# Kernel optimization log

Measured on AMD Instinct MI355X. Metric: run time of the kernel, lower is better.

## Reference

```python
import jax, jax.numpy as jnp
import numpy as np

U = 512  # units

def hard_sigmoid(x):
    # Keras hard_sigmoid: clip(0.2*x + 0.5, 0, 1)
    return jnp.clip(0.2 * x + 0.5, 0.0, 1.0)

def setup_inputs() -> dict:
    key = jax.random.key(0)
    ks = jax.random.split(key, 9)
    B, T, A, D = 64, 2048, 512, 512  # batch, annotation steps, annotation units, input dim
    s = lambda k, shape, scale: jax.random.normal(k, shape, jnp.float32) * scale
    return {
        "inputs": s(ks[0], (B, D), 1.0),
        "h": s(ks[1], (B, U), 1.0),
        "c": s(ks[2], (B, U), 1.0),
        "annotations": s(ks[3], (B, T, A), 1.0),
        "kernel": s(ks[4], (D + A, 4 * U), 0.02),
        "recurrent_kernel": s(ks[5], (U, 4 * U), 0.02),
        "bias": jnp.zeros((6 * U,), jnp.float32).at[U:2 * U].set(1.0),  # unit_forget_bias
        "kernel_u": s(ks[6], (A, U), 0.02),
        "kernel_w": s(ks[7], (U, U), 0.02),
        "kernel_v": s(ks[8], (U,), 0.02),
    }

def reference(inputs, h, c, annotations, kernel, recurrent_kernel, bias, kernel_u, kernel_w, kernel_v):
    bias_u = bias[4 * U:5 * U]
    # precomputed annotation projection (done once in build()): [B,T,U]
    uh = jnp.einsum('bta,au->btu', annotations, kernel_u) + bias_u
    # Bahdanau attention scores
    Wxstm = h @ kernel_w                                   # [B,U]
    et = jnp.einsum('btu,u->bt', jnp.tanh(uh + Wxstm[:, None, :]), kernel_v)
    at = jax.nn.softmax(et, axis=1)                        # exp/sum in source == softmax
    context = jnp.einsum('bt,bta->ba', at, annotations)    # [B,A]
    x = jnp.concatenate([inputs, context], axis=-1)        # [B, D+A]
    z = x @ kernel + h @ recurrent_kernel + bias[:4 * U]   # [B,4U]
    i = hard_sigmoid(z[:, :U])
    f = hard_sigmoid(z[:, U:2 * U])
    c_new = f * c + i * jnp.tanh(z[:, 2 * U:3 * U])
    o = hard_sigmoid(z[:, 3 * U:])
    h_new = o * jnp.tanh(c_new)
    return h_new
```

## Files before the change

### kernel.cpp

```cpp
#include <hip/hip_runtime.h>

constexpr int U = 512;
constexpr int B = 64;
constexpr int T = 2048;
constexpr int A = 512;

typedef __attribute__((ext_vector_type(8))) short short8;
typedef __attribute__((ext_vector_type(4))) float f32x4;

__device__ __forceinline__ unsigned short f32_to_bf16(float f) {
    unsigned int b = __float_as_uint(f);
    unsigned int r = (b + 0x7FFFu + ((b >> 16) & 1u)) >> 16;
    return (unsigned short)r;
}

__device__ __forceinline__ float fast_tanh(float x) {
    float e = exp2f(x * 2.885390081777927f);
    return (e - 1.0f) * __builtin_amdgcn_rcpf(e + 1.0f);
}

__device__ __forceinline__ float hard_sigmoid(float z) {
    return fminf(fmaxf(0.2f * z + 0.5f, 0.0f), 1.0f);
}

__global__ __launch_bounds__(256) void k_prep_s(const float* __restrict__ h,
                                                const float* __restrict__ kw,
                                                float* __restrict__ Sp) {
    int b = blockIdx.x >> 2;
    int kc = blockIdx.x & 3;
    int u = threadIdx.x;
    const float* hb = h + b * U + kc * 128;
    const float* kwb = kw + (size_t)kc * 128 * U;
    float a0 = 0.f, a1 = 0.f;
#pragma unroll 4
    for (int k = 0; k < 128; ++k) {
        float hv = hb[k];
        a0 += hv * kwb[(size_t)k * U + u];
        a1 += hv * kwb[(size_t)k * U + u + 256];
    }
    float* p = Sp + ((size_t)kc * 64 + b) * U;
    p[u] = a0;
    p[u + 256] = a1;
}

__global__ __launch_bounds__(256) void k_s_reduce(const float* __restrict__ Sp,
                                                  const float* __restrict__ bias,
                                                  float* __restrict__ S) {
    int gid = blockIdx.x * 256 + threadIdx.x;
    int b = gid >> 9, u = gid & 511;
    float s = bias[4 * U + u];
#pragma unroll
    for (int kc = 0; kc < 4; ++kc) s += Sp[((size_t)kc * 64 + b) * U + u];
    S[gid] = s;
}

__global__ __launch_bounds__(256) void k_prep_kut(const float* __restrict__ ku,
                                                  unsigned short* __restrict__ kut) {
    __shared__ float tile[32][33];
    int a0 = (blockIdx.x >> 4) << 5;
    int u0 = (blockIdx.x & 15) << 5;
    int c = threadIdx.x & 31, r0 = threadIdx.x >> 5;
#pragma unroll
    for (int p = 0; p < 4; ++p) {
        int r = r0 + p * 8;
        tile[r][c] = ku[(a0 + r) * U + u0 + c];
    }
    __syncthreads();
#pragma unroll
    for (int p = 0; p < 4; ++p) {
        int r = r0 + p * 8;
        kut[(u0 + r) * A + a0 + c] = f32_to_bf16(tile[c][r]);
    }
}

__global__ __launch_bounds__(256) void k_prep_wt(const float* __restrict__ kern,
                                                 const float* __restrict__ rk,
                                                 unsigned short* __restrict__ Wt) {
    __shared__ float tile[32][33];
    int k0 = blockIdx.x << 5;
    int j0 = blockIdx.y << 5;
    int c = threadIdx.x & 31, r0 = threadIdx.x >> 5;
#pragma unroll
    for (int p = 0; p < 4; ++p) {
        int r = r0 + p * 8;
        int k = k0 + r;
        float val = (k < 1024) ? kern[k * 2048 + j0 + c]
                               : rk[(k - 1024) * 2048 + j0 + c];
        tile[r][c] = val;
    }
    __syncthreads();
#pragma unroll
    for (int p = 0; p < 4; ++p) {
        int r = r0 + p * 8;
        Wt[(size_t)(j0 + r) * 1536 + k0 + c] = f32_to_bf16(tile[c][r]);
    }
}

__global__ __launch_bounds__(256, 2) void k_gemm_et(const float* __restrict__ ann,
                                                    const unsigned short* __restrict__ kut,
                                                    const float* __restrict__ S,
                                                    const float* __restrict__ v,
                                                    float* __restrict__ et) {
    __shared__ unsigned short As[2][64 * 32];
    __shared__ unsigned short Bs[2][512 * 32];
    __shared__ float red[4][64];

    const int tid = threadIdx.x;
    const int wave = tid >> 6;
    const int lane = tid & 63;
    const int lanelo = lane & 15;
    const int quad = lane >> 4;
    const int wn = wave;

    const int mt = blockIdx.x;
    const int b = mt >> 5;
    const int t0 = (mt & 31) << 6;
    const float* aBase = ann + (size_t)mt * 64 * A;

    f32x4 acc[4][8];
#pragma unroll
    for (int i = 0; i < 4; ++i)
#pragma unroll
        for (int j = 0; j < 8; ++j) acc[i][j] = {0.f, 0.f, 0.f, 0.f};

    const int rowA = tid >> 2;
    const int c8A = tid & 3;
    f32x4 pv0, pv1;

    {
        const float* src = aBase + (size_t)rowA * A + 0 + c8A * 8;
        pv0 = *(const f32x4*)src;
        pv1 = *(const f32x4*)(src + 4);
    }
#pragma unroll
    for (int p = 0; p < 8; ++p) {
        int seg = p * 4 + wave;
        int flat = seg * 1024 + lane * 16;
        int row = flat >> 6;
        int sc = (flat >> 4) & 3;
        int d = sc ^ ((row >> 1) & 3);
        __builtin_amdgcn_global_load_lds(
            (const __attribute__((address_space(1))) void*)(kut + (size_t)row * A + 0 + d * 8),
            (__attribute__((address_space(3))) void*)((char*)&Bs[0][0] + seg * 1024),
            16, 0, 0);
    }
    {
        short8 pk;
        pk[0] = (short)f32_to_bf16(pv0.x);
        pk[1] = (short)f32_to_bf16(pv0.y);
        pk[2] = (short)f32_to_bf16(pv0.z);
        pk[3] = (short)f32_to_bf16(pv0.w);
        pk[4] = (short)f32_to_bf16(pv1.x);
        pk[5] = (short)f32_to_bf16(pv1.y);
        pk[6] = (short)f32_to_bf16(pv1.z);
        pk[7] = (short)f32_to_bf16(pv1.w);
        *(short8*)&As[0][rowA * 32 + ((c8A ^ ((rowA >> 1) & 3)) * 8)] = pk;
    }
    __syncthreads();

    for (int t = 0; t < 16; ++t) {
        const int cur = t & 1;
        const int nxt = cur ^ 1;
        const bool more = (t < 15);
        const int k1 = (t + 1) * 32;

        if (more) {
            const float* src = aBase + (size_t)rowA * A + k1 + c8A * 8;
            pv0 = *(const f32x4*)src;
            pv1 = *(const f32x4*)(src + 4);
#pragma unroll
            for (int p = 0; p < 8; ++p) {
                int seg = p * 4 + wave;
                int flat = seg * 1024 + lane * 16;
                int row = flat >> 6;
                int sc = (flat >> 4) & 3;
                int d = sc ^ ((row >> 1) & 3);
                __builtin_amdgcn_global_load_lds(
                    (const __attribute__((address_space(1))) void*)(kut + (size_t)row * A + k1 + d * 8),
                    (__attribute__((address_space(3))) void*)((char*)&Bs[nxt][0] + seg * 1024),
                    16, 0, 0);
            }
        }

        short8 af[4];
#pragma unroll
        for (int mi = 0; mi < 4; ++mi) {
            int row = mi * 16 + lanelo;
            af[mi] = *(const short8*)&As[cur][row * 32 + ((quad ^ ((row >> 1) & 3)) * 8)];
        }
        short8 bfr[8];
#pragma unroll
        for (int ni = 0; ni < 8; ++ni) {
            int rowb = wn * 128 + ni * 16 + lanelo;
            bfr[ni] = *(const short8*)&Bs[cur][rowb * 32 + ((quad ^ ((rowb >> 1) & 3)) * 8)];
        }
        __builtin_amdgcn_s_setprio(1);
#pragma unroll
        for (int mi = 0; mi < 4; ++mi)
#pragma unroll
            for (int ni = 0; ni < 8; ++ni)
                acc[mi][ni] = __builtin_amdgcn_mfma_f32_16x16x32_bf16(
                    af[mi], bfr[ni], acc[mi][ni], 0, 0, 0);
        __builtin_amdgcn_s_setprio(0);

        if (more) {
            short8 pk;
            pk[0] = (short)f32_to_bf16(pv0.x);
            pk[1] = (short)f32_to_bf16(pv0.y);
            pk[2] = (short)f32_to_bf16(pv0.z);
            pk[3] = (short)f32_to_bf16(pv0.w);
            pk[4] = (short)f32_to_bf16(pv1.x);
            pk[5] = (short)f32_to_bf16(pv1.y);
            pk[6] = (short)f32_to_bf16(pv1.z);
            pk[7] = (short)f32_to_bf16(pv1.w);
            *(short8*)&As[nxt][rowA * 32 + ((c8A ^ ((rowA >> 1) & 3)) * 8)] = pk;
        }
        __syncthreads();
    }

    float rows[16];
#pragma unroll
    for (int i = 0; i < 16; ++i) rows[i] = 0.f;
#pragma unroll
    for (int ni = 0; ni < 8; ++ni) {
        int u = wn * 128 + ni * 16 + lanelo;
        float sv = S[b * U + u];
        float vv = v[u];
#pragma unroll
        for (int mi = 0; mi < 4; ++mi)
#pragma unroll
            for (int r = 0; r < 4; ++r)
                rows[mi * 4 + r] += fast_tanh(acc[mi][ni][r] + sv) * vv;
    }
#pragma unroll
    for (int i = 0; i < 16; ++i) {
        rows[i] += __shfl_xor(rows[i], 1);
        rows[i] += __shfl_xor(rows[i], 2);
        rows[i] += __shfl_xor(rows[i], 4);
        rows[i] += __shfl_xor(rows[i], 8);
    }
    if (lanelo == 0) {
#pragma unroll
        for (int mi = 0; mi < 4; ++mi)
#pragma unroll
            for (int r = 0; r < 4; ++r)
                red[wave][mi * 16 + quad * 4 + r] = rows[mi * 4 + r];
    }
    __syncthreads();
    if (tid < 64) {
        float sum = red[0][tid] + red[1][tid] + red[2][tid] + red[3][tid];
        et[b * T + t0 + tid] = sum;
    }
}

__global__ __launch_bounds__(256) void k_softmax(const float* __restrict__ et,
                                                 float* __restrict__ at) {
    __shared__ float sred[256];
    int b = blockIdx.x;
    const float* e = et + b * T;
    float vals[8];
    float mx = -1e30f;
#pragma unroll
    for (int i = 0; i < 8; ++i) {
        int t = threadIdx.x + i * 256;
        float x = e[t];
        vals[i] = x;
        mx = fmaxf(mx, x);
    }
    sred[threadIdx.x] = mx;
    __syncthreads();
    for (int s = 128; s > 0; s >>= 1) {
        if (threadIdx.x < s) sred[threadIdx.x] = fmaxf(sred[threadIdx.x], sred[threadIdx.x + s]);
        __syncthreads();
    }
    mx = sred[0];
    __syncthreads();
    float sum = 0.f;
#pragma unroll
    for (int i = 0; i < 8; ++i) {
        float x = exp2f((vals[i] - mx) * 1.4426950408889634f);
        vals[i] = x;
        sum += x;
    }
    sred[threadIdx.x] = sum;
    __syncthreads();
    for (int s = 128; s > 0; s >>= 1) {
        if (threadIdx.x < s) sred[threadIdx.x] += sred[threadIdx.x + s];
        __syncthreads();
    }
    float inv = 1.0f / sred[0];
#pragma unroll
    for (int i = 0; i < 8; ++i) at[b * T + threadIdx.x + i * 256] = vals[i] * inv;
}

__global__ __launch_bounds__(256) void k_ctx_part(const float* __restrict__ at,
                                                  const float* __restrict__ ann,
                                                  float* __restrict__ part) {
    __shared__ float buf[2][512];
    int b = blockIdx.x >> 3;
    int tc = blockIdx.x & 7;
    int half = threadIdx.x >> 7;
    int a4 = (threadIdx.x & 127) << 2;
    const float* annb = ann + ((size_t)b * T + tc * 256) * A;
    const float* atb = at + b * T + tc * 256;
    f32x4 acc = {0.f, 0.f, 0.f, 0.f};
    for (int t = half; t < 256; t += 2) {
        float w = atb[t];
        f32x4 rv = *(const f32x4*)(annb + (size_t)t * A + a4);
        acc.x += w * rv.x;
        acc.y += w * rv.y;
        acc.z += w * rv.z;
        acc.w += w * rv.w;
    }
    *(f32x4*)&buf[half][a4] = acc;
    __syncthreads();
    int a2 = threadIdx.x << 1;
    float s0 = buf[0][a2] + buf[1][a2];
    float s1 = buf[0][a2 + 1] + buf[1][a2 + 1];
    float* p = part + ((size_t)b * 8 + tc) * A;
    p[a2] = s0;
    p[a2 + 1] = s1;
}

__global__ __launch_bounds__(256) void k_ctx_xb(const float* __restrict__ part,
                                                const float* __restrict__ inputs,
                                                const float* __restrict__ h,
                                                unsigned short* __restrict__ xb) {
    int b = blockIdx.x;
    unsigned short* xrow = xb + (size_t)b * 1536;
#pragma unroll
    for (int i = 0; i < 2; ++i) {
        int a = threadIdx.x + i * 256;
        float s = 0.f;
#pragma unroll
        for (int c = 0; c < 8; ++c) s += part[((size_t)b * 8 + c) * A + a];
        xrow[512 + a] = f32_to_bf16(s);
        xrow[a] = f32_to_bf16(inputs[b * 512 + a]);
        xrow[1024 + a] = f32_to_bf16(h[b * 512 + a]);
    }
}

__global__ __launch_bounds__(256) void k_zgemm(const unsigned short* __restrict__ xb,
                                               const unsigned short* __restrict__ Wt,
                                               float* __restrict__ zpart) {
    const int kc = blockIdx.x & 7;
    const int nt = blockIdx.x >> 3;
    const int wave = threadIdx.x >> 6;
    const int lane = threadIdx.x & 63;
    const int lanelo = lane & 15;
    const int quad = lane >> 4;

    const int n = nt * 64 + wave * 16 + lanelo;
    const unsigned short* bp = Wt + (size_t)n * 1536 + kc * 192 + quad * 8;
    const unsigned short* ap = xb + (size_t)lanelo * 1536 + kc * 192 + quad * 8;

    f32x4 acc[4];
#pragma unroll
    for (int i = 0; i < 4; ++i) acc[i] = {0.f, 0.f, 0.f, 0.f};

#pragma unroll
    for (int ks = 0; ks < 6; ++ks) {
        short8 bfrag = *(const short8*)(bp + ks * 32);
#pragma unroll
        for (int mi = 0; mi < 4; ++mi) {
            short8 afrag = *(const short8*)(ap + (size_t)mi * 16 * 1536 + ks * 32);
            acc[mi] = __builtin_amdgcn_mfma_f32_16x16x32_bf16(afrag, bfrag, acc[mi], 0, 0, 0);
        }
    }

    float* p = zpart + (size_t)kc * 64 * 2048;
#pragma unroll
    for (int mi = 0; mi < 4; ++mi)
#pragma unroll
        for (int r = 0; r < 4; ++r) {
            int m = mi * 16 + quad * 4 + r;
            p[(size_t)m * 2048 + n] = acc[mi][r];
        }
}

__global__ __launch_bounds__(256) void k_gates(const float* __restrict__ zpart,
                                               const float* __restrict__ bias,
                                               const float* __restrict__ c,
                                               float* __restrict__ hnew) {
    int gid = blockIdx.x * 256 + threadIdx.x;
    int b = gid >> 9;
    int u = gid & 511;
    float z[4];
#pragma unroll
    for (int g = 0; g < 4; ++g) {
        int j = (g << 9) + u;
        float s = bias[j];
#pragma unroll
        for (int kc = 0; kc < 8; ++kc)
            s += zpart[((size_t)kc * 64 + b) * 2048 + j];
        z[g] = s;
    }
    float ig = hard_sigmoid(z[0]);
    float fg = hard_sigmoid(z[1]);
    float cn = fg * c[b * 512 + u] + ig * fast_tanh(z[2]);
    float og = hard_sigmoid(z[3]);
    hnew[b * 512 + u] = og * fast_tanh(cn);
}

extern "C" void kernel_launch(void* const* d_in, const int* in_sizes, int n_in,
                              void* d_out, int out_size, void* d_ws, size_t ws_size,
                              hipStream_t stream) {
    const float* inputs = (const float*)d_in[0];
    const float* h      = (const float*)d_in[1];
    const float* c      = (const float*)d_in[2];
    const float* ann    = (const float*)d_in[3];
    const float* kern   = (const float*)d_in[4];
    const float* rk     = (const float*)d_in[5];
    const float* bias   = (const float*)d_in[6];
    const float* ku     = (const float*)d_in[7];
    const float* kw     = (const float*)d_in[8];
    const float* kv     = (const float*)d_in[9];

    char* ws = (char*)d_ws;
    float*          S     = (float*)(ws + 0);
    unsigned short* kut   = (unsigned short*)(ws + 131072);
    float*          et    = (float*)(ws + 655360);
    float*          at    = (float*)(ws + 1703936);
    float*          part  = (float*)(ws + 2228224);
    float*          Sp    = (float*)(ws + 2228224);
    unsigned short* xb    = (unsigned short*)(ws + 3407872);
    unsigned short* Wt    = (unsigned short*)(ws + 3604480);
    float*          zpart = (float*)(ws + 9895936);
    float*          hnew  = (float*)d_out;

    k_prep_wt<<<dim3(48, 64), 256, 0, stream>>>(kern, rk, Wt);
    k_prep_kut<<<256, 256, 0, stream>>>(ku, kut);
    k_prep_s<<<256, 256, 0, stream>>>(h, kw, Sp);
    k_s_reduce<<<128, 256, 0, stream>>>(Sp, bias, S);
    k_gemm_et<<<2048, 256, 0, stream>>>(ann, kut, S, kv, et);
    k_softmax<<<64, 256, 0, stream>>>(et, at);
    k_ctx_part<<<64 * 8, 256, 0, stream>>>(at, ann, part);
    k_ctx_xb<<<64, 256, 0, stream>>>(part, inputs, h, xb);
    k_zgemm<<<256, 256, 0, stream>>>(xb, Wt, zpart);
    k_gates<<<128, 256, 0, stream>>>(zpart, bias, c, hnew);
}
```

Before: 544.8 us.

## Enlarge attention GEMM tile to 128 rows with triple-buffered B pipeline

```diff
diff --git a/kernel.cpp b/kernel.cpp
--- a/kernel.cpp
+++ b/kernel.cpp
@@ -96,26 +96,26 @@
     }
 }
 
-__global__ __launch_bounds__(256, 2) void k_gemm_et(const float* __restrict__ ann,
+__global__ __launch_bounds__(512, 1) void k_gemm_et(const float* __restrict__ ann,
                                                     const unsigned short* __restrict__ kut,
                                                     const float* __restrict__ S,
                                                     const float* __restrict__ v,
                                                     float* __restrict__ et) {
-    __shared__ unsigned short As[2][64 * 32];
-    __shared__ unsigned short Bs[2][512 * 32];
-    __shared__ float red[4][64];
+    __shared__ unsigned short As[2][128 * 40];
+    __shared__ unsigned short Bs[3][512 * 32];
+    __shared__ float red[8][64];
 
     const int tid = threadIdx.x;
     const int wave = tid >> 6;
     const int lane = tid & 63;
     const int lanelo = lane & 15;
     const int quad = lane >> 4;
-    const int wn = wave;
+    const int wr = wave >> 2;
+    const int wc = wave & 3;
 
     const int mt = blockIdx.x;
-    const int b = mt >> 5;
-    const int t0 = (mt & 31) << 6;
-    const float* aBase = ann + (size_t)mt * 64 * A;
+    const int b = mt >> 4;
+    const float* aBase = ann + (size_t)mt * 128 * A;
 
     f32x4 acc[4][8];
 #pragma unroll
@@ -127,24 +127,22 @@
     const int c8A = tid & 3;
     f32x4 pv0, pv1;
 
-    {
-        const float* src = aBase + (size_t)rowA * A + 0 + c8A * 8;
-        pv0 = *(const f32x4*)src;
-        pv1 = *(const f32x4*)(src + 4);
-    }
-#pragma unroll
-    for (int p = 0; p < 8; ++p) {
-        int seg = p * 4 + wave;
-        int flat = seg * 1024 + lane * 16;
-        int row = flat >> 6;
-        int sc = (flat >> 4) & 3;
-        int d = sc ^ ((row >> 1) & 3);
-        __builtin_amdgcn_global_load_lds(
-            (const __attribute__((address_space(1))) void*)(kut + (size_t)row * A + 0 + d * 8),
-            (__attribute__((address_space(3))) void*)((char*)&Bs[0][0] + seg * 1024),
-            16, 0, 0);
-    }
-    {
+    auto stage_b = [&](int kk, int buf) {
+#pragma unroll
+        for (int p = 0; p < 4; ++p) {
+            int seg = p * 8 + wave;
+            int flat = seg * 1024 + lane * 16;
+            int row = flat >> 6;
+            int sc = (flat >> 4) & 3;
+            int d = sc ^ ((row >> 1) & 3);
+            __builtin_amdgcn_global_load_lds(
+                (const __attribute__((address_space(1))) void*)(kut + (size_t)row * A + kk + d * 8),
+                (__attribute__((address_space(3))) void*)((char*)&Bs[buf][0] + seg * 1024),
+                16, 0, 0);
+        }
+    };
+
+    auto cvt_store = [&](int buf) {
         short8 pk;
         pk[0] = (short)f32_to_bf16(pv0.x);
         pk[1] = (short)f32_to_bf16(pv0.y);
@@ -154,46 +152,55 @@
         pk[5] = (short)f32_to_bf16(pv1.y);
         pk[6] = (short)f32_to_bf16(pv1.z);
         pk[7] = (short)f32_to_bf16(pv1.w);
-        *(short8*)&As[0][rowA * 32 + ((c8A ^ ((rowA >> 1) & 3)) * 8)] = pk;
-    }
-    __syncthreads();
-
+        *(short8*)&As[buf][rowA * 40 + c8A * 8] = pk;
+    };
+
+    {
+        const float* src = aBase + (size_t)rowA * A + c8A * 8;
+        pv0 = *(const f32x4*)src;
+        pv1 = *(const f32x4*)(src + 4);
+    }
+    __builtin_amdgcn_sched_barrier(0);
+    stage_b(0, 0);
+    __builtin_amdgcn_sched_barrier(0);
+    asm volatile("s_waitcnt vmcnt(4)" ::: "memory");
+    cvt_store(0);
+    __builtin_amdgcn_sched_barrier(0);
+    stage_b(32, 1);
+    __builtin_amdgcn_sched_barrier(0);
+    asm volatile("s_waitcnt vmcnt(4)" ::: "memory");
+    asm volatile("s_waitcnt lgkmcnt(0)" ::: "memory");
+    __builtin_amdgcn_s_barrier();
+
+#pragma unroll
     for (int t = 0; t < 16; ++t) {
         const int cur = t & 1;
-        const int nxt = cur ^ 1;
-        const bool more = (t < 15);
-        const int k1 = (t + 1) * 32;
-
-        if (more) {
-            const float* src = aBase + (size_t)rowA * A + k1 + c8A * 8;
+        const int curB = t % 3;
+
+        __builtin_amdgcn_sched_barrier(0);
+        if (t < 15) {
+            const float* src = aBase + (size_t)rowA * A + (t + 1) * 32 + c8A * 8;
             pv0 = *(const f32x4*)src;
             pv1 = *(const f32x4*)(src + 4);
-#pragma unroll
-            for (int p = 0; p < 8; ++p) {
-                int seg = p * 4 + wave;
-                int flat = seg * 1024 + lane * 16;
-                int row = flat >> 6;
-                int sc = (flat >> 4) & 3;
-                int d = sc ^ ((row >> 1) & 3);
-                __builtin_amdgcn_global_load_lds(
-                    (const __attribute__((address_space(1))) void*)(kut + (size_t)row * A + k1 + d * 8),
-                    (__attribute__((address_space(3))) void*)((char*)&Bs[nxt][0] + seg * 1024),
-                    16, 0, 0);
-            }
-        }
+        }
+        __builtin_amdgcn_sched_barrier(0);
+        if (t < 14) stage_b((t + 2) * 32, (t + 2) % 3);
+        __builtin_amdgcn_sched_barrier(0);
 
         short8 af[4];
 #pragma unroll
         for (int mi = 0; mi < 4; ++mi) {
-            int row = mi * 16 + lanelo;
-            af[mi] = *(const short8*)&As[cur][row * 32 + ((quad ^ ((row >> 1) & 3)) * 8)];
+            int row = wr * 64 + mi * 16 + lanelo;
+            af[mi] = *(const short8*)&As[cur][row * 40 + quad * 8];
         }
         short8 bfr[8];
 #pragma unroll
         for (int ni = 0; ni < 8; ++ni) {
-            int rowb = wn * 128 + ni * 16 + lanelo;
-            bfr[ni] = *(const short8*)&Bs[cur][rowb * 32 + ((quad ^ ((rowb >> 1) & 3)) * 8)];
-        }
+            int rowb = wc * 128 + ni * 16 + lanelo;
+            int ch = quad ^ ((rowb >> 1) & 3);
+            bfr[ni] = *(const short8*)&Bs[curB][rowb * 32 + ch * 8];
+        }
+
         __builtin_amdgcn_s_setprio(1);
 #pragma unroll
         for (int mi = 0; mi < 4; ++mi)
@@ -202,20 +209,16 @@
                 acc[mi][ni] = __builtin_amdgcn_mfma_f32_16x16x32_bf16(
                     af[mi], bfr[ni], acc[mi][ni], 0, 0, 0);
         __builtin_amdgcn_s_setprio(0);
-
-        if (more) {
-            short8 pk;
-            pk[0] = (short)f32_to_bf16(pv0.x);
-            pk[1] = (short)f32_to_bf16(pv0.y);
-            pk[2] = (short)f32_to_bf16(pv0.z);
-            pk[3] = (short)f32_to_bf16(pv0.w);
-            pk[4] = (short)f32_to_bf16(pv1.x);
-            pk[5] = (short)f32_to_bf16(pv1.y);
-            pk[6] = (short)f32_to_bf16(pv1.z);
-            pk[7] = (short)f32_to_bf16(pv1.w);
-            *(short8*)&As[nxt][rowA * 32 + ((c8A ^ ((rowA >> 1) & 3)) * 8)] = pk;
-        }
-        __syncthreads();
+        __builtin_amdgcn_sched_barrier(0);
+
+        if (t < 15) {
+            if (t == 14) { asm volatile("s_waitcnt vmcnt(0)" ::: "memory"); }
+            else         { asm volatile("s_waitcnt vmcnt(4)" ::: "memory"); }
+            __builtin_amdgcn_sched_barrier(0);
+            cvt_store((t + 1) & 1);
+        }
+        asm volatile("s_waitcnt lgkmcnt(0)" ::: "memory");
+        __builtin_amdgcn_s_barrier();
     }
 
     float rows[16];
@@ -223,7 +226,7 @@
     for (int i = 0; i < 16; ++i) rows[i] = 0.f;
 #pragma unroll
     for (int ni = 0; ni < 8; ++ni) {
-        int u = wn * 128 + ni * 16 + lanelo;
+        int u = wc * 128 + ni * 16 + lanelo;
         float sv = S[b * U + u];
         float vv = v[u];
 #pragma unroll
@@ -247,9 +250,12 @@
                 red[wave][mi * 16 + quad * 4 + r] = rows[mi * 4 + r];
     }
     __syncthreads();
-    if (tid < 64) {
-        float sum = red[0][tid] + red[1][tid] + red[2][tid] + red[3][tid];
-        et[b * T + t0 + tid] = sum;
+    if (tid < 128) {
+        int wrr = tid >> 6;
+        int m = tid & 63;
+        float sum = red[wrr * 4 + 0][m] + red[wrr * 4 + 1][m] +
+                    red[wrr * 4 + 2][m] + red[wrr * 4 + 3][m];
+        et[b * T + (mt & 15) * 128 + wrr * 64 + m] = sum;
     }
 }
 
@@ -297,14 +303,15 @@
                                                   const float* __restrict__ ann,
                                                   float* __restrict__ part) {
     __shared__ float buf[2][512];
-    int b = blockIdx.x >> 3;
-    int tc = blockIdx.x & 7;
+    int b = blockIdx.x >> 4;
+    int tc = blockIdx.x & 15;
     int half = threadIdx.x >> 7;
     int a4 = (threadIdx.x & 127) << 2;
-    const float* annb = ann + ((size_t)b * T + tc * 256) * A;
-    const float* atb = at + b * T + tc * 256;
+    const float* annb = ann + ((size_t)b * T + tc * 128) * A;
+    const float* atb = at + b * T + tc * 128;
     f32x4 acc = {0.f, 0.f, 0.f, 0.f};
-    for (int t = half; t < 256; t += 2) {
+#pragma unroll 4
+    for (int t = half; t < 128; t += 2) {
         float w = atb[t];
         f32x4 rv = *(const f32x4*)(annb + (size_t)t * A + a4);
         acc.x += w * rv.x;
@@ -317,7 +324,7 @@
     int a2 = threadIdx.x << 1;
     float s0 = buf[0][a2] + buf[1][a2];
     float s1 = buf[0][a2 + 1] + buf[1][a2 + 1];
-    float* p = part + ((size_t)b * 8 + tc) * A;
+    float* p = part + ((size_t)b * 16 + tc) * A;
     p[a2] = s0;
     p[a2 + 1] = s1;
 }
@@ -333,7 +340,7 @@
         int a = threadIdx.x + i * 256;
         float s = 0.f;
 #pragma unroll
-        for (int c = 0; c < 8; ++c) s += part[((size_t)b * 8 + c) * A + a];
+        for (int c = 0; c < 16; ++c) s += part[((size_t)b * 16 + c) * A + a];
         xrow[512 + a] = f32_to_bf16(s);
         xrow[a] = f32_to_bf16(inputs[b * 512 + a]);
         xrow[1024 + a] = f32_to_bf16(h[b * 512 + a]);
@@ -421,20 +428,20 @@
     unsigned short* kut   = (unsigned short*)(ws + 131072);
     float*          et    = (float*)(ws + 655360);
     float*          at    = (float*)(ws + 1703936);
-    float*          part  = (float*)(ws + 2228224);
     float*          Sp    = (float*)(ws + 2228224);
     unsigned short* xb    = (unsigned short*)(ws + 3407872);
     unsigned short* Wt    = (unsigned short*)(ws + 3604480);
     float*          zpart = (float*)(ws + 9895936);
+    float*          part  = (float*)(ws + 14090240);
     float*          hnew  = (float*)d_out;
 
     k_prep_wt<<<dim3(48, 64), 256, 0, stream>>>(kern, rk, Wt);
     k_prep_kut<<<256, 256, 0, stream>>>(ku, kut);
     k_prep_s<<<256, 256, 0, stream>>>(h, kw, Sp);
     k_s_reduce<<<128, 256, 0, stream>>>(Sp, bias, S);
-    k_gemm_et<<<2048, 256, 0, stream>>>(ann, kut, S, kv, et);
+    k_gemm_et<<<1024, 512, 0, stream>>>(ann, kut, S, kv, et);
     k_softmax<<<64, 256, 0, stream>>>(et, at);
-    k_ctx_part<<<64 * 8, 256, 0, stream>>>(at, ann, part);
+    k_ctx_part<<<64 * 16, 256, 0, stream>>>(at, ann, part);
     k_ctx_xb<<<64, 256, 0, stream>>>(part, inputs, h, xb);
     k_zgemm<<<256, 256, 0, stream>>>(xb, Wt, zpart);
     k_gates<<<128, 256, 0, stream>>>(zpart, bias, c, hnew);
```

New measurement: 507.4 us. 1.07x faster.
